# Kernel optimization log

Measured on AMD Instinct MI355X. Metric: run time of the kernel, lower is better.

The kernel has to match this reference:

```python
import jax, jax.numpy as jnp
import numpy as np

A, B = 64, 128           # n_atoms, batch
EMBED, NG = 128, 50      # embed_dim, num_gaussians
RADIUS = 12.0
AVG = 60.0               # avg_atoms
N_HID = 2                # num_layers=4 -> 2 residual hidden linears


def setup_inputs() -> dict:
    key = jax.random.key(0)
    ks = jax.random.split(key, 24)
    T = jax.random.normal(ks[0], (A, A, B, EMBED), dtype=jnp.float32)
    mask = (jax.random.uniform(ks[1], (A, A, B, 1)) < 0.9).astype(jnp.float32)
    dist = jax.random.uniform(ks[2], (A, A, B), dtype=jnp.float32) * RADIUS
    v = jax.random.normal(ks[3], (A, A, B, 3), dtype=jnp.float32)
    vec_hat = v / (jnp.linalg.norm(v, axis=-1, keepdims=True) + 1e-8)

    def w(k, shape):
        s = 1.0 / np.sqrt(shape[0])
        return jax.random.uniform(k, shape, minval=-s, maxval=s, dtype=jnp.float32)

    params = {}
    for pfx, base in (("e", 4), ("f", 14)):
        params[pfx + "W_in"] = w(ks[base + 0], (EMBED, EMBED))
        params[pfx + "b_in"] = w(ks[base + 1], (EMBED,))
        params[pfx + "W_h"] = jnp.stack([w(ks[base + 2], (EMBED, EMBED)),
                                          w(ks[base + 3], (EMBED, EMBED))])
        params[pfx + "b_h"] = jnp.stack([w(ks[base + 4], (EMBED,)),
                                          w(ks[base + 5], (EMBED,))])
        params[pfx + "W_out"] = w(ks[base + 6], (EMBED, EMBED))
        params[pfx + "b_out"] = w(ks[base + 7], (EMBED,))
        params[pfx + "_rbf_w"] = w(ks[base + 8], (NG, EMBED))
        params[pfx + "_head_w"] = w(ks[base + 9], (EMBED, 1))
    return dict(T=T, mask=mask, dist=dist, vec_hat=vec_hat, **params)


def _resmlp(x, W_in, b_in, W_h, b_h, W_out, b_out):
    # input -> SiLU -> residual hidden blocks -> output (dropout=0)
    x = jax.nn.silu(x @ W_in + b_in)
    for i in range(N_HID):
        x = x + jax.nn.silu(x @ W_h[i] + b_h[i])
    return x @ W_out + b_out


def _rbf(dist, w_rbf):
    offset = jnp.linspace(0.0, RADIUS, NG, dtype=jnp.float32)
    step = RADIUS / (NG - 1)
    coeff = -0.5 / step ** 2
    smeared = jnp.exp(coeff * jnp.square(dist[..., None] - offset))  # [A,A,B,NG]
    return smeared @ w_rbf                                            # [A,A,B,EMBED]


def reference(T, mask, dist, vec_hat,
              eW_in, eb_in, eW_h, eb_h, eW_out, eb_out, e_rbf_w, e_head_w,
              fW_in, fb_in, fW_h, fb_h, fW_out, fb_out, f_rbf_w, f_head_w):
    e_feat = _resmlp(T, eW_in, eb_in, eW_h, eb_h, eW_out, eb_out) * _rbf(dist, e_rbf_w)
    f_feat = _resmlp(T, fW_in, fb_in, fW_h, fb_h, fW_out, fb_out) * _rbf(dist, f_rbf_w)
    e = e_feat @ e_head_w                    # [A,A,B,1]
    f = (f_feat @ f_head_w) * vec_hat        # [A,A,B,3]
    energy = jnp.sum(e * mask, axis=(0, 1)) / (AVG ** 2)  # [B,1]
    forces = jnp.sum(f * mask, axis=0) / AVG               # [A,B,3]
    return energy, forces
```

## Files before the change

kernel.cpp:

```cpp
#include <hip/hip_runtime.h>

#define A_DIM 64
#define B_DIM 128
#define E 128
#define NG 50
#define NROW (A_DIM*A_DIM*B_DIM)
#define TR 64
#define KS 136
#define SMS 72
#define WBLK 512
#define BR_STRIDE 147456
#define NOUT (B_DIM + A_DIM*B_DIM*3)
#define WLSCALE 64.0f
#define WLINV   0.015625f

using half8   = _Float16 __attribute__((ext_vector_type(8)));
using short8v = short __attribute__((ext_vector_type(8)));
using f32x16  = float __attribute__((ext_vector_type(16)));

__device__ __forceinline__ float silu_f(float x) {
  return x * __builtin_amdgcn_rcpf(1.0f + __expf(-x));
}
__device__ __forceinline__ short hbits(_Float16 h) {
  return (short)__builtin_bit_cast(unsigned short, h);
}

__device__ __forceinline__ void gemm_chunk32(
    const short* __restrict__ xh_, int xstr, int kcol,
    const short* __restrict__ wl_, int cidx,
    f32x16 acc[2], f32x16 accl[2], int l31, int l5)
{
  half8 bh[2], bl[2];
  #pragma unroll
  for (int s = 0; s < 2; ++s) {
    bh[s] = __builtin_bit_cast(half8,
              *(const short8v*)(wl_ + (size_t)(cidx * 16 + s) * WBLK));
    bl[s] = __builtin_bit_cast(half8,
              *(const short8v*)(wl_ + (size_t)(cidx * 16 + 2 + s) * WBLK));
  }
  #pragma unroll
  for (int rt = 0; rt < 2; ++rt) {
    const short* arow = xh_ + (rt * 32 + l31) * xstr + kcol + l5 * 8;
    #pragma unroll
    for (int s = 0; s < 2; ++s) {
      half8 a = __builtin_bit_cast(half8, *(const short8v*)(arow + s * 16));
      acc[rt]  = __builtin_amdgcn_mfma_f32_32x32x16_f16(a, bh[s], acc[rt],  0, 0, 0);
      accl[rt] = __builtin_amdgcn_mfma_f32_32x32x16_f16(a, bl[s], accl[rt], 0, 0, 0);
    }
  }
}

__global__ __launch_bounds__(256) void prep_weights(
    const float* __restrict__ eWin, const float* __restrict__ eWh,
    const float* __restrict__ eWout, const float* __restrict__ erbf,
    const float* __restrict__ fWin, const float* __restrict__ fWh,
    const float* __restrict__ fWout, const float* __restrict__ frbf,
    short* __restrict__ S, float* __restrict__ out)
{
  if (blockIdx.x >= 576) {
    int i = (blockIdx.x - 576) * 256 + threadIdx.x;
    if (i < NOUT) out[i] = 0.0f;
    return;
  }
  int o = blockIdx.x * 256 + threadIdx.x;
  int br = (o >= 73728) ? 1 : 0;
  int r = o - br * 73728;
  short* base = S + br * BR_STRIDE;
  float v; int cidx, n, kk;
  if (r < 65536) {
    int lay = r >> 14, idx = r & 16383;
    int k = idx >> 7; n = idx & 127;
    const float* W = (lay == 0) ? (br ? fWin : eWin)
                   : (lay == 3) ? (br ? fWout : eWout)
                   : ((br ? fWh : eWh) + (lay - 1) * 16384);
    v = W[k * 128 + n];
    cidx = lay * 4 + (k >> 5); kk = k & 31;
  } else {
    int rr = r - 65536;
    int k = rr >> 7; n = rr & 127;
    v = (k < NG) ? (br ? frbf : erbf)[k * 128 + n] : 0.0f;
    cidx = 16 + (k >> 5); kk = k & 31;
  }
  int blk = cidx * 16 + (n >> 5) * 4 + (kk >> 4);
  int idx2 = blk * WBLK + ((n & 31) + 32 * ((kk >> 3) & 1)) * 8 + (kk & 7);
  _Float16 wh = (_Float16)v;
  _Float16 wl = (_Float16)((v - (float)wh) * WLSCALE);
  base[idx2] = hbits(wh);
  base[idx2 + 2 * WBLK] = hbits(wl);
}

__global__ __launch_bounds__(256, 3) void fused_main(
    const float* __restrict__ T, const float* __restrict__ mask,
    const float* __restrict__ dist, const float* __restrict__ vh,
    const float* __restrict__ ebin, const float* __restrict__ ebh,
    const float* __restrict__ ebout, const float* __restrict__ ehead,
    const float* __restrict__ fbin, const float* __restrict__ fbh,
    const float* __restrict__ fbout, const float* __restrict__ fhead,
    const short* __restrict__ S,
    float* __restrict__ out)
{
  __shared__ short xa[TR * KS];
  __shared__ float part[4][TR];

  const int t = threadIdx.x;
  const int wave = t >> 6, lane = t & 63;
  const int l31 = lane & 31, l5 = lane >> 5;
  const int br = blockIdx.x & 1;
  const long tile = blockIdx.x >> 1;
  const long r0g = tile * TR;

  const short* wl = S + br * BR_STRIDE + wave * (4 * WBLK) + lane * 8;
  const float* bin  = br ? fbin : ebin;
  const float* bh_  = br ? fbh : ebh;
  const float* bout = br ? fbout : ebout;
  const float* head = br ? fhead : ehead;

  {
    int row = t >> 2, seg = t & 3;
    const float* Tp = T + (r0g + row) * E + seg * 32;
    short* ph = xa + row * KS + seg * 32;
    #pragma unroll
    for (int j = 0; j < 8; ++j) {
      float4 v = *(const float4*)(Tp + j * 4);
      short4 s4 = make_short4(hbits((_Float16)v.x), hbits((_Float16)v.y),
                              hbits((_Float16)v.z), hbits((_Float16)v.w));
      *(short4*)(ph + j * 4) = s4;
    }
  }

  f32x16 acc[2], accl[2];

  #pragma unroll 1
  for (int lay = 0; lay < 4; ++lay) {
    const float* bg = (lay == 0) ? bin : (lay == 3) ? bout : (bh_ + (lay - 1) * E);
    float b0 = bg[wave * 32 + l31];
    #pragma unroll
    for (int i = 0; i < 16; ++i) {
      acc[0][i] = b0; acc[1][i] = b0;
      accl[0][i] = 0.f; accl[1][i] = 0.f;
    }
    __syncthreads();
    #pragma unroll
    for (int ch = 0; ch < 4; ++ch)
      gemm_chunk32(xa, KS, ch * 32, wl, lay * 4 + ch, acc, accl, l31, l5);
    __syncthreads();
    if (lay < 3) {
      #pragma unroll
      for (int rt = 0; rt < 2; ++rt)
        #pragma unroll
        for (int rg = 0; rg < 16; ++rg) {
          float y = acc[rt][rg] + accl[rt][rg] * WLINV;
          float v = silu_f(y);
          int rowa = rt * 32 + 4 * l5 + (rg & 3) + 8 * (rg >> 2);
          int col = wave * 32 + l31;
          short* slot = xa + rowa * KS + col;
          if (lay > 0) v += (float)*(const _Float16*)slot;
          *slot = hbits((_Float16)v);
        }
    }
  }
  #pragma unroll
  for (int rt = 0; rt < 2; ++rt)
    #pragma unroll
    for (int i = 0; i < 16; ++i) acc[rt][i] += accl[rt][i] * WLINV;

  short* smhi = xa;
  const float stepv = 12.0f / 49.0f;
  const float coeff = -0.5f / (stepv * stepv);
  {
    int r = t & 63, kg = t >> 6;
    float d = dist[r0g + r];
    #pragma unroll
    for (int j4 = 0; j4 < 4; ++j4) {
      float vv[4];
      #pragma unroll
      for (int jj = 0; jj < 4; ++jj) {
        int k = kg * 16 + j4 * 4 + jj;
        float dd = d - (float)k * stepv;
        vv[jj] = (k < NG) ? __expf(coeff * dd * dd) : 0.0f;
      }
      short4 s4 = make_short4(hbits((_Float16)vv[0]), hbits((_Float16)vv[1]),
                              hbits((_Float16)vv[2]), hbits((_Float16)vv[3]));
      *(short4*)(smhi + r * SMS + kg * 16 + j4 * 4) = s4;
    }
  }
  float h0 = head[wave * 32 + l31];
  f32x16 acc2[2], acc2l[2];
  #pragma unroll
  for (int i = 0; i < 16; ++i) {
    acc2[0][i] = 0.f; acc2[1][i] = 0.f;
    acc2l[0][i] = 0.f; acc2l[1][i] = 0.f;
  }
  __syncthreads();
  gemm_chunk32(smhi, SMS, 0,  wl, 16, acc2, acc2l, l31, l5);
  gemm_chunk32(smhi, SMS, 32, wl, 17, acc2, acc2l, l31, l5);

  #pragma unroll
  for (int rt = 0; rt < 2; ++rt)
    #pragma unroll
    for (int rg = 0; rg < 16; ++rg) {
      float rb = acc2[rt][rg] + acc2l[rt][rg] * WLINV;
      float p = acc[rt][rg] * rb * h0;
      p += __shfl_xor(p, 1); p += __shfl_xor(p, 2);
      p += __shfl_xor(p, 4); p += __shfl_xor(p, 8);
      p += __shfl_xor(p, 16);
      if (l31 == 0)
        part[wave][rt * 32 + 4 * l5 + (rg & 3) + 8 * (rg >> 2)] = p;
    }
  __syncthreads();
  if (t < TR) {
    long g = r0g + t;
    float pr = part[0][t] + part[1][t] + part[2][t] + part[3][t];
    float pm = pr * mask[g];
    if (br == 0) {
      atomicAdd(out + (int)(g & 127), pm * (1.0f / 3600.0f));
    } else {
      int b = (int)(g & 127);
      int j = (int)((g >> 7) & 63);
      float s = pm * (1.0f / 60.0f);
      float* fo = out + B_DIM + (j * B_DIM + b) * 3;
      atomicAdd(fo + 0, s * vh[g * 3 + 0]);
      atomicAdd(fo + 1, s * vh[g * 3 + 1]);
      atomicAdd(fo + 2, s * vh[g * 3 + 2]);
    }
  }
}

extern "C" void kernel_launch(void* const* d_in, const int* in_sizes, int n_in,
                              void* d_out, int out_size, void* d_ws, size_t ws_size,
                              hipStream_t stream) {
  const float* T    = (const float*)d_in[0];
  const float* mask = (const float*)d_in[1];
  const float* dist = (const float*)d_in[2];
  const float* vh   = (const float*)d_in[3];
  const float* eWin = (const float*)d_in[4];
  const float* ebin = (const float*)d_in[5];
  const float* eWh  = (const float*)d_in[6];
  const float* ebh  = (const float*)d_in[7];
  const float* eWout= (const float*)d_in[8];
  const float* ebout= (const float*)d_in[9];
  const float* erbf = (const float*)d_in[10];
  const float* ehead= (const float*)d_in[11];
  const float* fWin = (const float*)d_in[12];
  const float* fbin = (const float*)d_in[13];
  const float* fWh  = (const float*)d_in[14];
  const float* fbh  = (const float*)d_in[15];
  const float* fWout= (const float*)d_in[16];
  const float* fbout= (const float*)d_in[17];
  const float* frbf = (const float*)d_in[18];
  const float* fhead= (const float*)d_in[19];

  short* S = (short*)d_ws;
  float* out = (float*)d_out;

  prep_weights<<<576 + (NOUT + 255) / 256, 256, 0, stream>>>(
      eWin, eWh, eWout, erbf, fWin, fWh, fWout, frbf, S, out);
  fused_main<<<2 * (NROW / TR), 256, 0, stream>>>(
      T, mask, dist, vh,
      ebin, ebh, ebout, ehead,
      fbin, fbh, fbout, fhead,
      S, out);
}
```

Baseline: 811.1 us.

## Process both branches per block, sharing T tile and RBF smear; prefetch weights

Each block now handles both the energy and force MLP branches for its row tile instead of one, so the T tile is loaded and converted to fp16 once and the Gaussian smear is computed once and kept in its own LDS buffer. The residual stream is kept in fp32 registers rather than re-read from fp16 LDS, and weight fragments for the next chunk are prefetched while the current chunk's MFMAs run. This halves the grid and the global reads of T and dist, and drops some syncs. In exchange it uses more LDS and more registers (xres, separate tc/xb/sm buffers), which may lower occupancy, and each block runs twice as long.

```diff
diff --git a/kernel.cpp b/kernel.cpp
--- a/kernel.cpp
+++ b/kernel.cpp
@@ -25,28 +25,31 @@
   return (short)__builtin_bit_cast(unsigned short, h);
 }
 
-__device__ __forceinline__ void gemm_chunk32(
-    const short* __restrict__ xh_, int xstr, int kcol,
-    const short* __restrict__ wl_, int cidx,
-    f32x16 acc[2], f32x16 accl[2], int l31, int l5)
+struct WFrag { half8 h0, h1, l0, l1; };
+
+__device__ __forceinline__ WFrag load_wfrag(const short* __restrict__ wlb, int cidx) {
+  const short* p = wlb + (size_t)cidx * (16 * WBLK);
+  WFrag w;
+  w.h0 = __builtin_bit_cast(half8, *(const short8v*)(p + 0 * WBLK));
+  w.h1 = __builtin_bit_cast(half8, *(const short8v*)(p + 1 * WBLK));
+  w.l0 = __builtin_bit_cast(half8, *(const short8v*)(p + 2 * WBLK));
+  w.l1 = __builtin_bit_cast(half8, *(const short8v*)(p + 3 * WBLK));
+  return w;
+}
+
+__device__ __forceinline__ void gemm_w(
+    const short* __restrict__ xsrc, int xstr, int kcol,
+    const WFrag& w, f32x16 acc[2], f32x16 accl[2], int l31, int l5)
 {
-  half8 bh[2], bl[2];
-  #pragma unroll
-  for (int s = 0; s < 2; ++s) {
-    bh[s] = __builtin_bit_cast(half8,
-              *(const short8v*)(wl_ + (size_t)(cidx * 16 + s) * WBLK));
-    bl[s] = __builtin_bit_cast(half8,
-              *(const short8v*)(wl_ + (size_t)(cidx * 16 + 2 + s) * WBLK));
-  }
   #pragma unroll
   for (int rt = 0; rt < 2; ++rt) {
-    const short* arow = xh_ + (rt * 32 + l31) * xstr + kcol + l5 * 8;
-    #pragma unroll
-    for (int s = 0; s < 2; ++s) {
-      half8 a = __builtin_bit_cast(half8, *(const short8v*)(arow + s * 16));
-      acc[rt]  = __builtin_amdgcn_mfma_f32_32x32x16_f16(a, bh[s], acc[rt],  0, 0, 0);
-      accl[rt] = __builtin_amdgcn_mfma_f32_32x32x16_f16(a, bl[s], accl[rt], 0, 0, 0);
-    }
+    const short* arow = xsrc + (rt * 32 + l31) * xstr + kcol + l5 * 8;
+    half8 a0 = __builtin_bit_cast(half8, *(const short8v*)arow);
+    half8 a1 = __builtin_bit_cast(half8, *(const short8v*)(arow + 16));
+    acc[rt]  = __builtin_amdgcn_mfma_f32_32x32x16_f16(a0, w.h0, acc[rt],  0, 0, 0);
+    accl[rt] = __builtin_amdgcn_mfma_f32_32x32x16_f16(a0, w.l0, accl[rt], 0, 0, 0);
+    acc[rt]  = __builtin_amdgcn_mfma_f32_32x32x16_f16(a1, w.h1, acc[rt],  0, 0, 0);
+    accl[rt] = __builtin_amdgcn_mfma_f32_32x32x16_f16(a1, w.l1, accl[rt], 0, 0, 0);
   }
 }
 
@@ -99,26 +102,20 @@
     const short* __restrict__ S,
     float* __restrict__ out)
 {
-  __shared__ short xa[TR * KS];
+  __shared__ short tc[TR * KS];
+  __shared__ short xb[TR * KS];
+  __shared__ short sm[TR * SMS];
   __shared__ float part[4][TR];
 
   const int t = threadIdx.x;
   const int wave = t >> 6, lane = t & 63;
   const int l31 = lane & 31, l5 = lane >> 5;
-  const int br = blockIdx.x & 1;
-  const long tile = blockIdx.x >> 1;
-  const long r0g = tile * TR;
-
-  const short* wl = S + br * BR_STRIDE + wave * (4 * WBLK) + lane * 8;
-  const float* bin  = br ? fbin : ebin;
-  const float* bh_  = br ? fbh : ebh;
-  const float* bout = br ? fbout : ebout;
-  const float* head = br ? fhead : ehead;
+  const long r0g = (long)blockIdx.x * TR;
 
   {
     int row = t >> 2, seg = t & 3;
     const float* Tp = T + (r0g + row) * E + seg * 32;
-    short* ph = xa + row * KS + seg * 32;
+    short* ph = tc + row * KS + seg * 32;
     #pragma unroll
     for (int j = 0; j < 8; ++j) {
       float4 v = *(const float4*)(Tp + j * 4);
@@ -127,47 +124,9 @@
       *(short4*)(ph + j * 4) = s4;
     }
   }
-
-  f32x16 acc[2], accl[2];
-
-  #pragma unroll 1
-  for (int lay = 0; lay < 4; ++lay) {
-    const float* bg = (lay == 0) ? bin : (lay == 3) ? bout : (bh_ + (lay - 1) * E);
-    float b0 = bg[wave * 32 + l31];
-    #pragma unroll
-    for (int i = 0; i < 16; ++i) {
-      acc[0][i] = b0; acc[1][i] = b0;
-      accl[0][i] = 0.f; accl[1][i] = 0.f;
-    }
-    __syncthreads();
-    #pragma unroll
-    for (int ch = 0; ch < 4; ++ch)
-      gemm_chunk32(xa, KS, ch * 32, wl, lay * 4 + ch, acc, accl, l31, l5);
-    __syncthreads();
-    if (lay < 3) {
-      #pragma unroll
-      for (int rt = 0; rt < 2; ++rt)
-        #pragma unroll
-        for (int rg = 0; rg < 16; ++rg) {
-          float y = acc[rt][rg] + accl[rt][rg] * WLINV;
-          float v = silu_f(y);
-          int rowa = rt * 32 + 4 * l5 + (rg & 3) + 8 * (rg >> 2);
-          int col = wave * 32 + l31;
-          short* slot = xa + rowa * KS + col;
-          if (lay > 0) v += (float)*(const _Float16*)slot;
-          *slot = hbits((_Float16)v);
-        }
-    }
-  }
-  #pragma unroll
-  for (int rt = 0; rt < 2; ++rt)
-    #pragma unroll
-    for (int i = 0; i < 16; ++i) acc[rt][i] += accl[rt][i] * WLINV;
-
-  short* smhi = xa;
-  const float stepv = 12.0f / 49.0f;
-  const float coeff = -0.5f / (stepv * stepv);
   {
+    const float stepv = 12.0f / 49.0f;
+    const float coeff = -0.5f / (stepv * stepv);
     int r = t & 63, kg = t >> 6;
     float d = dist[r0g + r];
     #pragma unroll
@@ -181,47 +140,98 @@
       }
       short4 s4 = make_short4(hbits((_Float16)vv[0]), hbits((_Float16)vv[1]),
                               hbits((_Float16)vv[2]), hbits((_Float16)vv[3]));
-      *(short4*)(smhi + r * SMS + kg * 16 + j4 * 4) = s4;
-    }
-  }
-  float h0 = head[wave * 32 + l31];
-  f32x16 acc2[2], acc2l[2];
-  #pragma unroll
-  for (int i = 0; i < 16; ++i) {
-    acc2[0][i] = 0.f; acc2[1][i] = 0.f;
-    acc2l[0][i] = 0.f; acc2l[1][i] = 0.f;
-  }
-  __syncthreads();
-  gemm_chunk32(smhi, SMS, 0,  wl, 16, acc2, acc2l, l31, l5);
-  gemm_chunk32(smhi, SMS, 32, wl, 17, acc2, acc2l, l31, l5);
-
-  #pragma unroll
-  for (int rt = 0; rt < 2; ++rt)
-    #pragma unroll
-    for (int rg = 0; rg < 16; ++rg) {
-      float rb = acc2[rt][rg] + acc2l[rt][rg] * WLINV;
-      float p = acc[rt][rg] * rb * h0;
-      p += __shfl_xor(p, 1); p += __shfl_xor(p, 2);
-      p += __shfl_xor(p, 4); p += __shfl_xor(p, 8);
-      p += __shfl_xor(p, 16);
-      if (l31 == 0)
-        part[wave][rt * 32 + 4 * l5 + (rg & 3) + 8 * (rg >> 2)] = p;
-    }
-  __syncthreads();
-  if (t < TR) {
-    long g = r0g + t;
-    float pr = part[0][t] + part[1][t] + part[2][t] + part[3][t];
-    float pm = pr * mask[g];
-    if (br == 0) {
-      atomicAdd(out + (int)(g & 127), pm * (1.0f / 3600.0f));
-    } else {
-      int b = (int)(g & 127);
-      int j = (int)((g >> 7) & 63);
-      float s = pm * (1.0f / 60.0f);
-      float* fo = out + B_DIM + (j * B_DIM + b) * 3;
-      atomicAdd(fo + 0, s * vh[g * 3 + 0]);
-      atomicAdd(fo + 1, s * vh[g * 3 + 1]);
-      atomicAdd(fo + 2, s * vh[g * 3 + 2]);
+      *(short4*)(sm + r * SMS + kg * 16 + j4 * 4) = s4;
+    }
+  }
+
+  #pragma unroll 1
+  for (int br2 = 0; br2 < 2; ++br2) {
+    const short* wlb = S + br2 * BR_STRIDE + wave * (4 * WBLK) + lane * 8;
+    const float* bin  = br2 ? fbin : ebin;
+    const float* bh_  = br2 ? fbh : ebh;
+    const float* bout = br2 ? fbout : ebout;
+    const float* head = br2 ? fhead : ehead;
+
+    WFrag wc = load_wfrag(wlb, 0);
+    f32x16 acc[2], accl[2];
+    float xres[2][16];
+
+    #pragma unroll 1
+    for (int lay = 0; lay < 4; ++lay) {
+      const float* bg = (lay == 0) ? bin : (lay == 3) ? bout : (bh_ + (lay - 1) * E);
+      float b0 = bg[wave * 32 + l31];
+      #pragma unroll
+      for (int i = 0; i < 16; ++i) {
+        acc[0][i] = b0; acc[1][i] = b0;
+        accl[0][i] = 0.f; accl[1][i] = 0.f;
+      }
+      __syncthreads();
+      const short* xsrc = (lay == 0) ? tc : xb;
+      #pragma unroll
+      for (int ch = 0; ch < 4; ++ch) {
+        WFrag wn = load_wfrag(wlb, lay * 4 + ch + 1);
+        gemm_w(xsrc, KS, ch * 32, wc, acc, accl, l31, l5);
+        wc = wn;
+      }
+      if (lay < 3) {
+        __syncthreads();
+        #pragma unroll
+        for (int rt = 0; rt < 2; ++rt)
+          #pragma unroll
+          for (int rg = 0; rg < 16; ++rg) {
+            float y = acc[rt][rg] + accl[rt][rg] * WLINV;
+            float v = silu_f(y);
+            if (lay > 0) v += xres[rt][rg];
+            xres[rt][rg] = v;
+            int rowa = rt * 32 + 4 * l5 + (rg & 3) + 8 * (rg >> 2);
+            xb[rowa * KS + wave * 32 + l31] = hbits((_Float16)v);
+          }
+      }
+    }
+    #pragma unroll
+    for (int rt = 0; rt < 2; ++rt)
+      #pragma unroll
+      for (int i = 0; i < 16; ++i) acc[rt][i] += accl[rt][i] * WLINV;
+
+    WFrag w17 = load_wfrag(wlb, 17);
+    f32x16 acc2[2], acc2l[2];
+    #pragma unroll
+    for (int i = 0; i < 16; ++i) {
+      acc2[0][i] = 0.f; acc2[1][i] = 0.f;
+      acc2l[0][i] = 0.f; acc2l[1][i] = 0.f;
+    }
+    gemm_w(sm, SMS, 0,  wc,  acc2, acc2l, l31, l5);
+    gemm_w(sm, SMS, 32, w17, acc2, acc2l, l31, l5);
+
+    float h0 = head[wave * 32 + l31];
+    #pragma unroll
+    for (int rt = 0; rt < 2; ++rt)
+      #pragma unroll
+      for (int rg = 0; rg < 16; ++rg) {
+        float rb = acc2[rt][rg] + acc2l[rt][rg] * WLINV;
+        float p = acc[rt][rg] * rb * h0;
+        p += __shfl_xor(p, 1); p += __shfl_xor(p, 2);
+        p += __shfl_xor(p, 4); p += __shfl_xor(p, 8);
+        p += __shfl_xor(p, 16);
+        if (l31 == 0)
+          part[wave][rt * 32 + 4 * l5 + (rg & 3) + 8 * (rg >> 2)] = p;
+      }
+    __syncthreads();
+    if (t < TR) {
+      long g = r0g + t;
+      float pr = part[0][t] + part[1][t] + part[2][t] + part[3][t];
+      float pm = pr * mask[g];
+      if (br2 == 0) {
+        atomicAdd(out + (int)(g & 127), pm * (1.0f / 3600.0f));
+      } else {
+        int b = (int)(g & 127);
+        int j = (int)((g >> 7) & 63);
+        float s = pm * (1.0f / 60.0f);
+        float* fo = out + B_DIM + (j * B_DIM + b) * 3;
+        atomicAdd(fo + 0, s * vh[g * 3 + 0]);
+        atomicAdd(fo + 1, s * vh[g * 3 + 1]);
+        atomicAdd(fo + 2, s * vh[g * 3 + 2]);
+      }
     }
   }
 }
@@ -255,7 +265,7 @@
 
   prep_weights<<<576 + (NOUT + 255) / 256, 256, 0, stream>>>(
       eWin, eWh, eWout, erbf, fWin, fWh, fWout, frbf, S, out);
-  fused_main<<<2 * (NROW / TR), 256, 0, stream>>>(
+  fused_main<<<NROW / TR, 256, 0, stream>>>(
       T, mask, dist, vh,
       ebin, ebh, ebout, ehead,
       fbin, fbh, fbout, fhead,
```

New measurement: 1.813 ms. +123.5%, slower.
